# Optimization experiments

Measured on AMD Instinct MI355X. Metric: run time of the kernel, lower is better.

Reference implementation:

```python
import jax, jax.numpy as jnp
import numpy as np

D_IN = 256
D_ATTN = 64
STEPS = 2
TOP_P = 0.9
TAU = 1.0
LN_EPS = 1e-5
N_NODES = 8192


def setup_inputs() -> dict:
    key = jax.random.key(0)
    ks = jax.random.split(key, 8)
    N, d, da, steps = N_NODES, D_IN, D_ATTN, STEPS
    X = jax.random.normal(ks[0], (N, d), dtype=jnp.float32)
    S = jax.random.uniform(ks[1], (N, N), dtype=jnp.float32)
    # Linear weights stored torch-style: (out_features, in_features)
    W1 = jax.random.normal(ks[2], (da, d), dtype=jnp.float32) / np.sqrt(d)
    W2 = jax.random.normal(ks[3], (da, da), dtype=jnp.float32) / np.sqrt(da)
    W3 = jax.random.normal(ks[4], (da, d), dtype=jnp.float32) / np.sqrt(d)
    U1 = jax.random.normal(ks[5], (steps, d, d), dtype=jnp.float32) / np.sqrt(d)
    U2 = jax.random.normal(ks[6], (steps, d, d), dtype=jnp.float32) / np.sqrt(d)
    ln_g = jnp.ones((d,), dtype=jnp.float32)
    ln_b = jnp.zeros((d,), dtype=jnp.float32)
    return {"X": X, "S": S, "W1": W1, "W2": W2, "W3": W3,
            "U1": U1, "U2": U2, "ln_g": ln_g, "ln_b": ln_b}


def _top_p_attention(X, W1, W2, W3):
    """Bilinear attention adjacency with nucleus (top-p) sparsification.
    X: (N, d_in) -> A: (N, N) row-stochastic."""
    q = (X @ W1.T) @ W2.T                    # (N, d_attn)
    k = X @ W3.T                             # (N, d_attn)
    logits = (q @ k.T) / TAU                 # (N, N)
    probs = jax.nn.softmax(logits, axis=-1)
    idx = jnp.argsort(-probs, axis=-1)       # descending order indices
    sp = jnp.take_along_axis(probs, idx, axis=-1)
    cs = jnp.cumsum(sp, axis=-1)
    keep_sorted = (cs - sp) < TOP_P          # keep minimal prefix reaching mass p
    rows = jnp.arange(probs.shape[0])[:, None]
    mask = jnp.zeros(probs.shape, dtype=bool).at[rows, idx].set(keep_sorted)
    A = probs * mask
    return A / jnp.maximum(A.sum(-1, keepdims=True), 1e-12)


def reference(X, S, W1, W2, W3, U1, U2, ln_g, ln_b):
    N = X.shape[0]
    # prior: add self-loops, row-normalize
    R = S + jnp.eye(N, dtype=X.dtype)
    R = R / R.sum(-1, keepdims=True)
    Z = jnp.zeros_like(X)
    Xf = X
    Xa = X
    for n in range(STEPS):
        A = _top_p_attention(Xa, W1, W2, W3)
        Xf = R @ Xf                          # prior diffusion
        Xa = A @ Xa                          # adaptive diffusion
        # dropout is eval-mode identity
        Z = Z + Xf @ U1[n].T + Xa @ U2[n].T
    h = X + Z
    mu = h.mean(-1, keepdims=True)
    var = jnp.mean((h - mu) ** 2, axis=-1, keepdims=True)
    return (h - mu) / jnp.sqrt(var + LN_EPS) * ln_g + ln_b
```

## Files before the change

### kernel.cpp

```cpp
#include <hip/hip_runtime.h>
#include <stdint.h>

#define NN 8192
#define D 256
#define DA 64
#define CAND 2048

typedef unsigned short ushort_t;

__device__ float blockSumF(float v, float* scr) {
  __syncthreads();
#pragma unroll
  for (int o = 32; o > 0; o >>= 1) v += __shfl_down(v, o, 64);
  if ((threadIdx.x & 63) == 0) scr[threadIdx.x >> 6] = v;
  __syncthreads();
  return ((scr[0] + scr[1]) + (scr[2] + scr[3]));
}
__device__ float blockMaxF(float v, float* scr) {
  __syncthreads();
#pragma unroll
  for (int o = 32; o > 0; o >>= 1) v = fmaxf(v, __shfl_down(v, o, 64));
  if ((threadIdx.x & 63) == 0) scr[threadIdx.x >> 6] = v;
  __syncthreads();
  return fmaxf(fmaxf(scr[0], scr[1]), fmaxf(scr[2], scr[3]));
}
__device__ float blockScanIncl(float v, float* wscr) {
#pragma unroll
  for (int off = 1; off < 64; off <<= 1) {
    float u = __shfl_up(v, off, 64);
    if ((threadIdx.x & 63) >= off) v += u;
  }
  __syncthreads();
  if ((threadIdx.x & 63) == 63) wscr[threadIdx.x >> 6] = v;
  __syncthreads();
  float add = 0.0f;
  int wid = threadIdx.x >> 6;
  for (int w = 0; w < wid; w++) add += wscr[w];
  return v + add;
}

__global__ void zero_kernel(float* __restrict__ p, size_t n) {
  for (size_t i = (size_t)blockIdx.x * blockDim.x + threadIdx.x; i < n;
       i += (size_t)gridDim.x * blockDim.x)
    p[i] = 0.0f;
}

__global__ __launch_bounds__(256) void rowsum_kernel(const float* __restrict__ S, float* __restrict__ den) {
  __shared__ float scr[4];
  int row = blockIdx.x, tid = threadIdx.x;
  const float* sr = S + (size_t)row * NN;
  float s = 0;
  for (int c = tid * 4; c < NN; c += 1024) {
    float4 u = *(const float4*)(sr + c);
    s += (u.x + u.y) + (u.z + u.w);
  }
  float tot = blockSumF(s, scr);
  if (tid == 0) den[row] = tot + 1.0f;
}

__global__ __launch_bounds__(256) void xf_gemm(const float* __restrict__ S,
                                               const float* __restrict__ XfC,
                                               const float* __restrict__ den,
                                               float* __restrict__ XfN) {
  __shared__ float Ast[64][68];
  __shared__ float Bs[64][68];
  int tid = threadIdx.x;
  int tx = tid & 15, ty = tid >> 4;
  int rb = blockIdx.x * 64;
  int cb = blockIdx.y * 64;
  float acc[4][4] = {};
  for (int kt = 0; kt < NN; kt += 64) {
    for (int i = tid; i < 4096; i += 256) {
      int r = i >> 6, c = i & 63;
      Ast[c][r] = S[(size_t)(rb + r) * NN + kt + c];
      Bs[r][c] = XfC[(size_t)(kt + r) * D + cb + c];
    }
    __syncthreads();
#pragma unroll 8
    for (int k = 0; k < 64; k++) {
      float4 av = *(const float4*)&Ast[k][ty * 4];
      float4 bv = *(const float4*)&Bs[k][tx * 4];
      acc[0][0] = fmaf(av.x, bv.x, acc[0][0]); acc[0][1] = fmaf(av.x, bv.y, acc[0][1]);
      acc[0][2] = fmaf(av.x, bv.z, acc[0][2]); acc[0][3] = fmaf(av.x, bv.w, acc[0][3]);
      acc[1][0] = fmaf(av.y, bv.x, acc[1][0]); acc[1][1] = fmaf(av.y, bv.y, acc[1][1]);
      acc[1][2] = fmaf(av.y, bv.z, acc[1][2]); acc[1][3] = fmaf(av.y, bv.w, acc[1][3]);
      acc[2][0] = fmaf(av.z, bv.x, acc[2][0]); acc[2][1] = fmaf(av.z, bv.y, acc[2][1]);
      acc[2][2] = fmaf(av.z, bv.z, acc[2][2]); acc[2][3] = fmaf(av.z, bv.w, acc[2][3]);
      acc[3][0] = fmaf(av.w, bv.x, acc[3][0]); acc[3][1] = fmaf(av.w, bv.y, acc[3][1]);
      acc[3][2] = fmaf(av.w, bv.z, acc[3][2]); acc[3][3] = fmaf(av.w, bv.w, acc[3][3]);
    }
    __syncthreads();
  }
#pragma unroll
  for (int i = 0; i < 4; i++) {
    int r = rb + ty * 4 + i;
    float dinv = 1.0f / den[r];
#pragma unroll
    for (int j = 0; j < 4; j++) {
      int c = cb + tx * 4 + j;
      XfN[(size_t)r * D + c] = (acc[i][j] + XfC[(size_t)r * D + c]) * dinv;
    }
  }
}

__global__ __launch_bounds__(64) void qk32_kernel(const float* __restrict__ Xa,
    const float* __restrict__ W1, const float* __restrict__ W2, const float* __restrict__ W3,
    float* __restrict__ qf, float* __restrict__ kf) {
  __shared__ float x[D];
  __shared__ float ts[DA];
  int row = blockIdx.x, tid = threadIdx.x;
  for (int i = tid; i < D; i += 64) x[i] = Xa[(size_t)row * D + i];
  __syncthreads();
  const float* w1r = W1 + (size_t)tid * D;
  const float* w3r = W3 + (size_t)tid * D;
  float t = 0.0f, kv = 0.0f;
  for (int d = 0; d < D; d++) {
    float xv = x[d];
    t  = fmaf(xv, w1r[d], t);
    kv = fmaf(xv, w3r[d], kv);
  }
  kf[(size_t)row * DA + tid] = kv;
  ts[tid] = t;
  __syncthreads();
  const float* w2r = W2 + (size_t)tid * DA;
  float qv = 0.0f;
  for (int a = 0; a < DA; a++) qv = fmaf(ts[a], w2r[a], qv);
  qf[(size_t)row * DA + tid] = qv;
}

__global__ __launch_bounds__(256) void logits32(const float* __restrict__ qf,
    const float* __restrict__ kf, float* __restrict__ L, int rowBase) {
  __shared__ float qs[64][65];
  __shared__ float ks[64][65];
  int tid = threadIdx.x;
  int tx = tid & 15, ty = tid >> 4;
  int colTile = blockIdx.x * 64;
  int rowTile = blockIdx.y * 64;
  for (int i = tid; i < 4096; i += 256) {
    int r = i >> 6, c = i & 63;
    qs[c][r] = qf[(size_t)(rowBase + rowTile + r) * DA + c];
    ks[c][r] = kf[(size_t)(colTile + r) * DA + c];
  }
  __syncthreads();
  float acc[4][4] = {};
  for (int c = 0; c < 64; c++) {
    float a0 = qs[c][ty * 4], a1 = qs[c][ty * 4 + 1];
    float a2 = qs[c][ty * 4 + 2], a3 = qs[c][ty * 4 + 3];
    float b0 = ks[c][tx * 4], b1 = ks[c][tx * 4 + 1];
    float b2 = ks[c][tx * 4 + 2], b3 = ks[c][tx * 4 + 3];
    acc[0][0] = fmaf(a0, b0, acc[0][0]); acc[0][1] = fmaf(a0, b1, acc[0][1]);
    acc[0][2] = fmaf(a0, b2, acc[0][2]); acc[0][3] = fmaf(a0, b3, acc[0][3]);
    acc[1][0] = fmaf(a1, b0, acc[1][0]); acc[1][1] = fmaf(a1, b1, acc[1][1]);
    acc[1][2] = fmaf(a1, b2, acc[1][2]); acc[1][3] = fmaf(a1, b3, acc[1][3]);
    acc[2][0] = fmaf(a2, b0, acc[2][0]); acc[2][1] = fmaf(a2, b1, acc[2][1]);
    acc[2][2] = fmaf(a2, b2, acc[2][2]); acc[2][3] = fmaf(a2, b3, acc[2][3]);
    acc[3][0] = fmaf(a3, b0, acc[3][0]); acc[3][1] = fmaf(a3, b1, acc[3][1]);
    acc[3][2] = fmaf(a3, b2, acc[3][2]); acc[3][3] = fmaf(a3, b3, acc[3][3]);
  }
#pragma unroll
  for (int i = 0; i < 4; i++)
#pragma unroll
    for (int j = 0; j < 4; j++)
      L[(size_t)(rowTile + ty * 4 + i) * NN + colTile + tx * 4 + j] = acc[i][j];
}

__global__ __launch_bounds__(256) void topp_histsel(const float* __restrict__ L,
    const float* __restrict__ XaOld, float* __restrict__ XaNew, int rowBase) {
  __shared__ float ps[NN];
  __shared__ float hsum[256];
  __shared__ float hcntf[256];
  __shared__ float cv[CAND];
  __shared__ ushort_t ci[CAND];
  __shared__ float wsum[4][256];
  __shared__ float wscr[4];
  __shared__ float scr[4];
  __shared__ float zsh;
  __shared__ unsigned sh_lo, sh_hi, sh_tie;
  __shared__ float sh_M, sh_asum, sh_hs;
  __shared__ int sh_C, sh_cross, sh_hc, sh_icut, sh_nkt, sh_ntot, sh_cnt;

  int tid = threadIdx.x;
  const float* Lr = L + (size_t)blockIdx.x * NN;
  float lm = -INFINITY;
  for (int c = tid * 4; c < NN; c += 1024) {
    float4 u = *(const float4*)(Lr + c);
    ps[c] = u.x; ps[c + 1] = u.y; ps[c + 2] = u.z; ps[c + 3] = u.w;
    lm = fmaxf(fmaxf(lm, fmaxf(u.x, u.y)), fmaxf(u.z, u.w));
  }
  float m = blockMaxF(lm, scr);
  if (tid < 64) {
    int base = tid * 128;
    float r[8];
#pragma unroll
    for (int j = 0; j < 8; j++) r[j] = expf(ps[base + j] - m);
    for (int i = 8; i < 128; i += 8)
#pragma unroll
      for (int j = 0; j < 8; j++) r[j] += expf(ps[base + i + j] - m);
    float leaf = ((r[0] + r[1]) + (r[2] + r[3])) + ((r[4] + r[5]) + (r[6] + r[7]));
#pragma unroll
    for (int off = 1; off < 64; off <<= 1) leaf += __shfl_down(leaf, off, 64);
    if (tid == 0) zsh = leaf;
  }
  hsum[tid] = 0.0f; hcntf[tid] = 0.0f;
  if (tid == 0) { sh_M = 0.0f; sh_C = 0; sh_cross = 256; }
  __syncthreads();
  float z = zsh;
  for (int j = tid; j < NN; j += 256) {
    float p = expf(ps[j] - m) / z;
    ps[j] = p;
    int b = (int)(__float_as_uint(p) >> 20) - 768;
    if (b >= 0) { atomicAdd(&hsum[b], p); atomicAdd(&hcntf[b], 1.0f); }
  }
  __syncthreads();
  for (int lev = 0; lev < 4; lev++) {
    float x  = hsum[255 - tid];
    float xc = hcntf[255 - tid];
    float inclm = blockScanIncl(x, wscr);
    float inclc = blockScanIncl(xc, wscr);
    if (sh_M + inclm >= 0.9f) atomicMin(&sh_cross, tid);
    __syncthreads();
    int ct = sh_cross; if (ct == 256) ct = 255;
    if (tid == ct) {
      int key = 255 - tid;
      sh_M = sh_M + (inclm - x);
      sh_C = sh_C + (int)(inclc - xc + 0.5f);
      sh_hs = x; sh_hc = (int)(xc + 0.5f);
      unsigned nlo, nhi;
      if (lev == 0) { nlo = (unsigned)(768 + key) << 20; nhi = nlo + (1u << 20); }
      else {
        int s = (lev == 1) ? 12 : (lev == 2) ? 4 : 0;
        nlo = sh_lo + ((unsigned)key << s); nhi = nlo + (1u << s);
      }
      sh_lo = nlo; sh_hi = nhi;
    }
    __syncthreads();
    if (sh_hc == 1 || lev == 3) break;
    hsum[tid] = 0.0f; hcntf[tid] = 0.0f;
    if (tid == 0) sh_cross = 256;
    __syncthreads();
    unsigned rlo = sh_lo, rhi = sh_hi;
    int s2 = (lev == 0) ? 12 : (lev == 1) ? 4 : 0;
    unsigned msk = (lev == 2) ? 15u : 255u;
    for (int j = tid; j < NN; j += 256) {
      unsigned u = __float_as_uint(ps[j]);
      if (u >= rlo && u < rhi) {
        unsigned key = (u >> s2) & msk;
        atomicAdd(&hsum[key], ps[j]); atomicAdd(&hcntf[key], 1.0f);
      }
    }
    __syncthreads();
  }
  if (tid == 0) {
    if (sh_hc == 1) {
      sh_tie = sh_lo; sh_nkt = 1; sh_asum = sh_M + sh_hs; sh_icut = NN;
    } else {
      float tiev = __uint_as_float(sh_lo);
      float cs = sh_M; int n = 0; int nt = sh_hc;
      while (n < nt && cs < 0.9f) { cs += tiev; n++; }
      sh_tie = sh_lo; sh_nkt = n; sh_asum = cs;
      sh_icut = (n == nt) ? NN : ((n == 0) ? -1 : -2);
    }
    sh_ntot = sh_C + sh_nkt;
    sh_cnt = 0;
  }
  __syncthreads();
  if (sh_icut == -2) {
    int need = sh_nkt; unsigned tb = sh_tie;
    int lo_ = 0, hi_ = NN - 1;
    for (int it = 0; it < 13; it++) {
      int mid = (lo_ + hi_) >> 1;
      float c = 0.0f;
      for (int j = tid; j < NN; j += 256)
        if (__float_as_uint(ps[j]) == tb && j <= mid) c += 1.0f;
      c = blockSumF(c, scr);
      if (c >= (float)need) hi_ = mid; else lo_ = mid + 1;
    }
    if (tid == 0) sh_icut = hi_;
    __syncthreads();
  }
  unsigned tie = sh_tie; int icut = sh_icut;
  float asum = fmaxf(sh_asum, 1e-12f);
  int ntot = sh_ntot;
  int wid = tid >> 6, lane = tid & 63;
  float4 acc; acc.x = acc.y = acc.z = acc.w = 0.0f;
  if (ntot <= CAND) {
    for (int j = tid; j < NN; j += 256) {
      float p = ps[j]; unsigned u = __float_as_uint(p);
      if (u > tie || (u == tie && j <= icut)) {
        int s = atomicAdd(&sh_cnt, 1);
        cv[s] = p; ci[s] = (ushort_t)j;
      }
    }
    __syncthreads();
    int nc = sh_cnt;
    for (int i = wid; i < nc; i += 4) {
      float pw = cv[i] / asum;
      const float4 xv = *(const float4*)(XaOld + (size_t)ci[i] * D + lane * 4);
      acc.x = fmaf(pw, xv.x, acc.x); acc.y = fmaf(pw, xv.y, acc.y);
      acc.z = fmaf(pw, xv.z, acc.z); acc.w = fmaf(pw, xv.w, acc.w);
    }
  } else {
    for (int j = wid; j < NN; j += 4) {
      float p = ps[j]; unsigned u = __float_as_uint(p);
      if (u > tie || (u == tie && j <= icut)) {
        float pw = p / asum;
        const float4 xv = *(const float4*)(XaOld + (size_t)j * D + lane * 4);
        acc.x = fmaf(pw, xv.x, acc.x); acc.y = fmaf(pw, xv.y, acc.y);
        acc.z = fmaf(pw, xv.z, acc.z); acc.w = fmaf(pw, xv.w, acc.w);
      }
    }
    __syncthreads();
  }
  *(float4*)&wsum[wid][lane * 4] = acc;
  __syncthreads();
  int col = tid;
  float o = (wsum[0][col] + wsum[1][col]) + (wsum[2][col] + wsum[3][col]);
  XaNew[(size_t)(rowBase + blockIdx.x) * D + col] = o;
}

__global__ __launch_bounds__(256) void z_accum(const float* __restrict__ Xf, const float* __restrict__ Xa,
    const float* __restrict__ U1n, const float* __restrict__ U2n, float* __restrict__ Z) {
  __shared__ float xf[4][D];
  __shared__ float xa[4][D];
  int r0 = blockIdx.x * 4, tid = threadIdx.x;
  for (int i = tid; i < 4 * D; i += 256) {
    xf[i >> 8][i & 255] = Xf[(size_t)r0 * D + i];
    xa[i >> 8][i & 255] = Xa[(size_t)r0 * D + i];
  }
  __syncthreads();
  const float* u1r = U1n + (size_t)tid * D;
  const float* u2r = U2n + (size_t)tid * D;
  float a0 = 0, a1 = 0, a2 = 0, a3 = 0, b0 = 0, b1 = 0, b2 = 0, b3 = 0;
  for (int d = 0; d < D; d += 4) {
    float4 u1 = *(const float4*)(u1r + d);
    float4 u2 = *(const float4*)(u2r + d);
    float f1[4] = {u1.x, u1.y, u1.z, u1.w};
    float f2[4] = {u2.x, u2.y, u2.z, u2.w};
#pragma unroll
    for (int j = 0; j < 4; j++) {
      int dd = d + j;
      a0 += xf[0][dd] * f1[j]; a1 += xf[1][dd] * f1[j];
      a2 += xf[2][dd] * f1[j]; a3 += xf[3][dd] * f1[j];
      b0 += xa[0][dd] * f2[j]; b1 += xa[1][dd] * f2[j];
      b2 += xa[2][dd] * f2[j]; b3 += xa[3][dd] * f2[j];
    }
  }
  Z[(size_t)(r0 + 0) * D + tid] += a0 + b0;
  Z[(size_t)(r0 + 1) * D + tid] += a1 + b1;
  Z[(size_t)(r0 + 2) * D + tid] += a2 + b2;
  Z[(size_t)(r0 + 3) * D + tid] += a3 + b3;
}

__global__ __launch_bounds__(256) void ln_kernel(const float* __restrict__ X, const float* __restrict__ Z,
    const float* __restrict__ g, const float* __restrict__ bb, float* __restrict__ out) {
  __shared__ float scr[4];
  int row = blockIdx.x, tid = threadIdx.x;
  float h = X[(size_t)row * D + tid] + Z[(size_t)row * D + tid];
  float mu = blockSumF(h, scr) * (1.0f / 256.0f);
  float dv = h - mu;
  float var = blockSumF(dv * dv, scr) * (1.0f / 256.0f);
  float o = dv / sqrtf(var + 1e-5f) * g[tid] + bb[tid];
  out[(size_t)row * D + tid] = o;
}

extern "C" void kernel_launch(void* const* d_in, const int* in_sizes, int n_in,
                              void* d_out, int out_size, void* d_ws, size_t ws_size,
                              hipStream_t stream) {
  const float* X  = (const float*)d_in[0];
  const float* S  = (const float*)d_in[1];
  const float* W1 = (const float*)d_in[2];
  const float* W2 = (const float*)d_in[3];
  const float* W3 = (const float*)d_in[4];
  const float* U1 = (const float*)d_in[5];
  const float* U2 = (const float*)d_in[6];
  const float* g  = (const float*)d_in[7];
  const float* b  = (const float*)d_in[8];

  char* w = (char*)d_ws;
  size_t off = 0;
  auto alloc = [&](size_t bytes) {
    void* p = w + off; off += (bytes + 255) & ~(size_t)255; return p;
  };
  float* A1  = (float*)alloc((size_t)NN * D * 4);
  float* A2  = (float*)alloc((size_t)NN * D * 4);
  float* F1  = (float*)alloc((size_t)NN * D * 4);
  float* F2  = (float*)alloc((size_t)NN * D * 4);
  float* Z   = (float*)alloc((size_t)NN * D * 4);
  float* den = (float*)alloc((size_t)NN * 4);
  float* qf  = (float*)alloc((size_t)NN * DA * 4);
  float* kf  = (float*)alloc((size_t)NN * DA * 4);
  int chunk = 512;
  while (chunk > 64 && off + (size_t)chunk * NN * 4 + 4096 > ws_size) chunk >>= 1;
  float* L32 = (float*)alloc((size_t)chunk * NN * 4);
  (void)in_sizes; (void)n_in; (void)out_size;

  zero_kernel<<<1024, 256, 0, stream>>>(Z, (size_t)NN * D);
  rowsum_kernel<<<NN, 256, 0, stream>>>(S, den);

  const float* XaC = X;  float* XaN = A1;
  const float* XfC = X;  float* XfN = F1;
  for (int n = 0; n < 2; n++) {
    xf_gemm<<<dim3(128, 4), 256, 0, stream>>>(S, XfC, den, XfN);
    qk32_kernel<<<NN, 64, 0, stream>>>(XaC, W1, W2, W3, qf, kf);
    for (int c = 0; c < NN / chunk; c++) {
      logits32<<<dim3(NN / 64, chunk / 64), 256, 0, stream>>>(qf, kf, L32, c * chunk);
      topp_histsel<<<chunk, 256, 0, stream>>>(L32, XaC, XaN, c * chunk);
    }
    z_accum<<<2048, 256, 0, stream>>>(XfN, XaN, U1 + (size_t)n * D * D, U2 + (size_t)n * D * D, Z);
    XaC = XaN; XaN = A2;
    XfC = XfN; XfN = F2;
  }
  ln_kernel<<<NN, 256, 0, stream>>>(X, Z, g, b, (float*)d_out);
}
```

Measured before the change: 6.081 ms.

## Split-K the prior GEMM and streamline top-p softmax and gather

Result: faster. 5.213 ms (-14.3%).

```diff
diff --git a/kernel.cpp b/kernel.cpp
--- a/kernel.cpp
+++ b/kernel.cpp
@@ -58,18 +58,18 @@
   if (tid == 0) den[row] = tot + 1.0f;
 }
 
-__global__ __launch_bounds__(256) void xf_gemm(const float* __restrict__ S,
-                                               const float* __restrict__ XfC,
-                                               const float* __restrict__ den,
-                                               float* __restrict__ XfN) {
+__global__ __launch_bounds__(256) void xf_gemm_sk(const float* __restrict__ S,
+                                                  const float* __restrict__ XfC,
+                                                  float* __restrict__ XfN) {
   __shared__ float Ast[64][68];
   __shared__ float Bs[64][68];
   int tid = threadIdx.x;
   int tx = tid & 15, ty = tid >> 4;
   int rb = blockIdx.x * 64;
   int cb = blockIdx.y * 64;
+  int k0 = blockIdx.z * (NN / 2);
   float acc[4][4] = {};
-  for (int kt = 0; kt < NN; kt += 64) {
+  for (int kt = k0; kt < k0 + NN / 2; kt += 64) {
     for (int i = tid; i < 4096; i += 256) {
       int r = i >> 6, c = i & 63;
       Ast[c][r] = S[(size_t)(rb + r) * NN + kt + c];
@@ -94,13 +94,26 @@
 #pragma unroll
   for (int i = 0; i < 4; i++) {
     int r = rb + ty * 4 + i;
-    float dinv = 1.0f / den[r];
 #pragma unroll
     for (int j = 0; j < 4; j++) {
       int c = cb + tx * 4 + j;
-      XfN[(size_t)r * D + c] = (acc[i][j] + XfC[(size_t)r * D + c]) * dinv;
-    }
-  }
+      atomicAdd(&XfN[(size_t)r * D + c], acc[i][j]);
+    }
+  }
+}
+
+__global__ __launch_bounds__(256) void xf_combine(float* __restrict__ XfN,
+                                                  const float* __restrict__ XfC,
+                                                  const float* __restrict__ den) {
+  size_t i4 = ((size_t)blockIdx.x * 256 + threadIdx.x) * 4;
+  int r = (int)(i4 >> 8);
+  float dinv = 1.0f / den[r];
+  float4 a = *(const float4*)(XfN + i4);
+  float4 x = *(const float4*)(XfC + i4);
+  float4 o;
+  o.x = (a.x + x.x) * dinv; o.y = (a.y + x.y) * dinv;
+  o.z = (a.z + x.z) * dinv; o.w = (a.w + x.w) * dinv;
+  *(float4*)(XfN + i4) = o;
 }
 
 __global__ __launch_bounds__(64) void qk32_kernel(const float* __restrict__ Xa,
@@ -174,56 +187,53 @@
   __shared__ float wsum[4][256];
   __shared__ float wscr[4];
   __shared__ float scr[4];
-  __shared__ float zsh;
   __shared__ unsigned sh_lo, sh_hi, sh_tie;
   __shared__ float sh_M, sh_asum, sh_hs;
-  __shared__ int sh_C, sh_cross, sh_hc, sh_icut, sh_nkt, sh_ntot, sh_cnt;
+  __shared__ int sh_cross, sh_hc, sh_icut, sh_nkt, sh_cnt;
 
   int tid = threadIdx.x;
   const float* Lr = L + (size_t)blockIdx.x * NN;
   float lm = -INFINITY;
   for (int c = tid * 4; c < NN; c += 1024) {
     float4 u = *(const float4*)(Lr + c);
-    ps[c] = u.x; ps[c + 1] = u.y; ps[c + 2] = u.z; ps[c + 3] = u.w;
+    *(float4*)(ps + c) = u;
     lm = fmaxf(fmaxf(lm, fmaxf(u.x, u.y)), fmaxf(u.z, u.w));
   }
   float m = blockMaxF(lm, scr);
-  if (tid < 64) {
-    int base = tid * 128;
-    float r[8];
-#pragma unroll
-    for (int j = 0; j < 8; j++) r[j] = expf(ps[base + j] - m);
-    for (int i = 8; i < 128; i += 8)
-#pragma unroll
-      for (int j = 0; j < 8; j++) r[j] += expf(ps[base + i + j] - m);
-    float leaf = ((r[0] + r[1]) + (r[2] + r[3])) + ((r[4] + r[5]) + (r[6] + r[7]));
-#pragma unroll
-    for (int off = 1; off < 64; off <<= 1) leaf += __shfl_down(leaf, off, 64);
-    if (tid == 0) zsh = leaf;
-  }
   hsum[tid] = 0.0f; hcntf[tid] = 0.0f;
-  if (tid == 0) { sh_M = 0.0f; sh_C = 0; sh_cross = 256; }
-  __syncthreads();
-  float z = zsh;
-  for (int j = tid; j < NN; j += 256) {
-    float p = expf(ps[j] - m) / z;
-    ps[j] = p;
-    int b = (int)(__float_as_uint(p) >> 20) - 768;
-    if (b >= 0) { atomicAdd(&hsum[b], p); atomicAdd(&hcntf[b], 1.0f); }
-  }
-  __syncthreads();
+  if (tid == 0) { sh_M = 0.0f; sh_cross = 256; }
+  __syncthreads();
+  float zp = 0.0f;
+  for (int c = tid * 4; c < NN; c += 1024) {
+    float4 u = *(const float4*)(ps + c);
+    float4 ev;
+    ev.x = expf(u.x - m); ev.y = expf(u.y - m);
+    ev.z = expf(u.z - m); ev.w = expf(u.w - m);
+    *(float4*)(ps + c) = ev;
+    zp += (ev.x + ev.y) + (ev.z + ev.w);
+    int b0 = (int)(__float_as_uint(ev.x) >> 20) - 768;
+    if (b0 >= 0) { atomicAdd(&hsum[b0], ev.x); atomicAdd(&hcntf[b0], 1.0f); }
+    int b1 = (int)(__float_as_uint(ev.y) >> 20) - 768;
+    if (b1 >= 0) { atomicAdd(&hsum[b1], ev.y); atomicAdd(&hcntf[b1], 1.0f); }
+    int b2 = (int)(__float_as_uint(ev.z) >> 20) - 768;
+    if (b2 >= 0) { atomicAdd(&hsum[b2], ev.z); atomicAdd(&hcntf[b2], 1.0f); }
+    int b3 = (int)(__float_as_uint(ev.w) >> 20) - 768;
+    if (b3 >= 0) { atomicAdd(&hsum[b3], ev.w); atomicAdd(&hcntf[b3], 1.0f); }
+  }
+  float Z = blockSumF(zp, scr);
+  float thr = 0.9f * Z;
   for (int lev = 0; lev < 4; lev++) {
     float x  = hsum[255 - tid];
     float xc = hcntf[255 - tid];
     float inclm = blockScanIncl(x, wscr);
     float inclc = blockScanIncl(xc, wscr);
-    if (sh_M + inclm >= 0.9f) atomicMin(&sh_cross, tid);
+    (void)inclc;
+    if (sh_M + inclm >= thr) atomicMin(&sh_cross, tid);
     __syncthreads();
     int ct = sh_cross; if (ct == 256) ct = 255;
     if (tid == ct) {
       int key = 255 - tid;
       sh_M = sh_M + (inclm - x);
-      sh_C = sh_C + (int)(inclc - xc + 0.5f);
       sh_hs = x; sh_hc = (int)(xc + 0.5f);
       unsigned nlo, nhi;
       if (lev == 0) { nlo = (unsigned)(768 + key) << 20; nhi = nlo + (1u << 20); }
@@ -256,12 +266,10 @@
     } else {
       float tiev = __uint_as_float(sh_lo);
       float cs = sh_M; int n = 0; int nt = sh_hc;
-      while (n < nt && cs < 0.9f) { cs += tiev; n++; }
+      while (n < nt && cs < thr) { cs += tiev; n++; }
       sh_tie = sh_lo; sh_nkt = n; sh_asum = cs;
       sh_icut = (n == nt) ? NN : ((n == 0) ? -1 : -2);
     }
-    sh_ntot = sh_C + sh_nkt;
-    sh_cnt = 0;
   }
   __syncthreads();
   if (sh_icut == -2) {
@@ -280,11 +288,12 @@
   }
   unsigned tie = sh_tie; int icut = sh_icut;
   float asum = fmaxf(sh_asum, 1e-12f);
-  int ntot = sh_ntot;
   int wid = tid >> 6, lane = tid & 63;
   float4 acc; acc.x = acc.y = acc.z = acc.w = 0.0f;
-  if (ntot <= CAND) {
-    for (int j = tid; j < NN; j += 256) {
+  for (int base = 0; base < NN; base += CAND) {
+    if (tid == 0) sh_cnt = 0;
+    __syncthreads();
+    for (int j = base + tid; j < base + CAND; j += 256) {
       float p = ps[j]; unsigned u = __float_as_uint(p);
       if (u > tie || (u == tie && j <= icut)) {
         int s = atomicAdd(&sh_cnt, 1);
@@ -293,21 +302,29 @@
     }
     __syncthreads();
     int nc = sh_cnt;
-    for (int i = wid; i < nc; i += 4) {
-      float pw = cv[i] / asum;
+    for (int s = tid; s < nc; s += 256) cv[s] = cv[s] / asum;
+    __syncthreads();
+    int i0 = (nc * wid) >> 2;
+    int i1 = (nc * (wid + 1)) >> 2;
+    int i = i0;
+    for (; i + 8 <= i1; i += 8) {
+      float pw[8]; float4 xr[8];
+#pragma unroll
+      for (int u = 0; u < 8; u++) {
+        pw[u] = cv[i + u];
+        xr[u] = *(const float4*)(XaOld + (size_t)ci[i + u] * D + lane * 4);
+      }
+#pragma unroll
+      for (int u = 0; u < 8; u++) {
+        acc.x = fmaf(pw[u], xr[u].x, acc.x); acc.y = fmaf(pw[u], xr[u].y, acc.y);
+        acc.z = fmaf(pw[u], xr[u].z, acc.z); acc.w = fmaf(pw[u], xr[u].w, acc.w);
+      }
+    }
+    for (; i < i1; i++) {
+      float pw = cv[i];
       const float4 xv = *(const float4*)(XaOld + (size_t)ci[i] * D + lane * 4);
       acc.x = fmaf(pw, xv.x, acc.x); acc.y = fmaf(pw, xv.y, acc.y);
       acc.z = fmaf(pw, xv.z, acc.z); acc.w = fmaf(pw, xv.w, acc.w);
-    }
-  } else {
-    for (int j = wid; j < NN; j += 4) {
-      float p = ps[j]; unsigned u = __float_as_uint(p);
-      if (u > tie || (u == tie && j <= icut)) {
-        float pw = p / asum;
-        const float4 xv = *(const float4*)(XaOld + (size_t)j * D + lane * 4);
-        acc.x = fmaf(pw, xv.x, acc.x); acc.y = fmaf(pw, xv.y, acc.y);
-        acc.z = fmaf(pw, xv.z, acc.z); acc.w = fmaf(pw, xv.w, acc.w);
-      }
     }
     __syncthreads();
   }
@@ -400,7 +417,9 @@
   const float* XaC = X;  float* XaN = A1;
   const float* XfC = X;  float* XfN = F1;
   for (int n = 0; n < 2; n++) {
-    xf_gemm<<<dim3(128, 4), 256, 0, stream>>>(S, XfC, den, XfN);
+    zero_kernel<<<1024, 256, 0, stream>>>(XfN, (size_t)NN * D);
+    xf_gemm_sk<<<dim3(NN / 64, D / 64, 2), 256, 0, stream>>>(S, XfC, XfN);
+    xf_combine<<<NN * D / 1024, 256, 0, stream>>>(XfN, XfC, den);
     qk32_kernel<<<NN, 64, 0, stream>>>(XaC, W1, W2, W3, qf, kf);
     for (int c = 0; c < NN / chunk; c++) {
       logits32<<<dim3(NN / 64, chunk / 64), 256, 0, stream>>>(qf, kf, L32, c * chunk);
```
